# Kernel optimization log

Hardware: AMD Instinct MI355X
Metric: run time of the kernel (lower is better)

## Reference

```python
import jax, jax.numpy as jnp
import numpy as np


def setup_inputs() -> dict:
    key = jax.random.key(0)
    k_h, k_w1, k_w2 = jax.random.split(key, 3)
    B, S, D = 8, 2048, 1024
    H = 2 * D  # reasoning_net hidden width
    # xavier_uniform-style scaled weights
    lim1 = float(np.sqrt(6.0 / (D + H)))
    lim2 = float(np.sqrt(6.0 / (H + D)))
    return {
        "hidden_states": jax.random.normal(k_h, (B, S, D), dtype=jnp.float32),
        "W1": jax.random.uniform(k_w1, (D, H), dtype=jnp.float32, minval=-lim1, maxval=lim1),
        "b1": jnp.zeros((H,), dtype=jnp.float32),
        "W2": jax.random.uniform(k_w2, (H, D), dtype=jnp.float32, minval=-lim2, maxval=lim2),
        "b2": jnp.zeros((D,), dtype=jnp.float32),
    }


def reference(hidden_states, W1, b1, W2, b2):
    """Chain reasoning forward.

    The torch loop carries output[:, -1:], but reasoning_net is a per-token MLP
    (Linear over the last dim), so processed[:, -1:] == MLP(current token) and the
    carried state never influences appended outputs. Faithful closed form:
      out[:, 0]  = hidden_states[:, 0]
      out[:, i]  = MLP(hidden_states[:, i])  for i >= 1
    Dropout is identity (eval). GELU is exact (torch default).
    """
    rest = hidden_states[:, 1:, :]  # [B, S-1, D]
    h = jax.nn.gelu(jnp.einsum("bsd,dh->bsh", rest, W1) + b1, approximate=False)
    out_rest = jnp.einsum("bsh,hd->bsd", h, W2) + b2
    return jnp.concatenate([hidden_states[:, :1, :], out_rest], axis=1)
```

## Files before the change

kernel.cpp:

```cpp
#include <hip/hip_runtime.h>
#include <hip/hip_bf16.h>
#include <cstdint>
#include <cstddef>

typedef unsigned short u16;
typedef __attribute__((ext_vector_type(8))) __bf16 bf16x8;
typedef __attribute__((ext_vector_type(4))) float f32x4;

__device__ __forceinline__ void gload_lds16(const void* g, void* l) {
    __builtin_amdgcn_global_load_lds(
        (const __attribute__((address_space(1))) unsigned int*)g,
        (__attribute__((address_space(3))) unsigned int*)l,
        16, 0, 0);
}

__device__ __forceinline__ u16 f2bf(float f) {
    union { float f; unsigned int u; } v; v.f = f;
    unsigned int r = v.u + 0x7fffu + ((v.u >> 16) & 1u);
    return (u16)(r >> 16);
}

template <int GELU, int OUT_BF16>
__global__ void gemm_bt_bias_act(const u16* __restrict__ A,
                                 const u16* __restrict__ Bt,
                                 const float* __restrict__ bias,
                                 void* __restrict__ Cv,
                                 int M, int N, int K) {
    __shared__ u16 As[128 * 32];
    __shared__ u16 Bs[128 * 32];

    const int tid  = threadIdx.x;
    const int lane = tid & 63;
    const int wave = tid >> 6;
    const int wm   = (wave >> 1) * 64;
    const int wn   = (wave & 1) * 64;
    const int mrow = lane & 15;
    const int half = lane >> 4;

    const size_t ldb = (size_t)K * 2;
    const char* Ab = (const char*)(A + (size_t)blockIdx.x * 128 * K);
    const char* Bb = (const char*)(Bt + (size_t)blockIdx.y * 128 * K);

    const int lin0 = tid, lin1 = tid + 256;
    const size_t aoff0 = (size_t)(lin0 >> 2) * ldb + ((lin0 & 3) << 4);
    const size_t aoff1 = (size_t)(lin1 >> 2) * ldb + ((lin1 & 3) << 4);

    f32x4 acc[4][4];
#pragma unroll
    for (int i = 0; i < 4; ++i)
#pragma unroll
        for (int j = 0; j < 4; ++j) acc[i][j] = f32x4{0.f, 0.f, 0.f, 0.f};

    for (int k0 = 0; k0 < K; k0 += 32) {
        const size_t kb = (size_t)k0 * 2;
        gload_lds16(Ab + aoff0 + kb, (char*)As + lin0 * 16);
        gload_lds16(Ab + aoff1 + kb, (char*)As + lin1 * 16);
        gload_lds16(Bb + aoff0 + kb, (char*)Bs + lin0 * 16);
        gload_lds16(Bb + aoff1 + kb, (char*)Bs + lin1 * 16);
        __syncthreads();

        bf16x8 af[4], bfr[4];
#pragma unroll
        for (int t = 0; t < 4; ++t)
            af[t] = *(const bf16x8*)(As + (wm + t * 16 + mrow) * 32 + half * 8);
#pragma unroll
        for (int t = 0; t < 4; ++t)
            bfr[t] = *(const bf16x8*)(Bs + (wn + t * 16 + mrow) * 32 + half * 8);

#pragma unroll
        for (int mi = 0; mi < 4; ++mi)
#pragma unroll
            for (int ni = 0; ni < 4; ++ni)
                acc[mi][ni] = __builtin_amdgcn_mfma_f32_16x16x32_bf16(
                    af[mi], bfr[ni], acc[mi][ni], 0, 0, 0);
        __syncthreads();
    }

    const int row0 = blockIdx.x * 128 + wm + half * 4;
    const int col0 = blockIdx.y * 128 + wn + mrow;
#pragma unroll
    for (int ni = 0; ni < 4; ++ni) {
        const int col = col0 + ni * 16;
        const float bv = bias[col];
#pragma unroll
        for (int mi = 0; mi < 4; ++mi) {
            const int row = row0 + mi * 16;
#pragma unroll
            for (int r = 0; r < 4; ++r) {
                float v = acc[mi][ni][r] + bv;
                if (GELU) v = 0.5f * v * (1.0f + erff(v * 0.70710678118654752f));
                if (OUT_BF16)
                    ((u16*)Cv)[(size_t)(row + r) * N + col] = f2bf(v);
                else
                    ((float*)Cv)[(size_t)(row + r) * N + col] = v;
            }
        }
    }
}

__global__ void transpose_cvt_bf16(const float* __restrict__ src,
                                   u16* __restrict__ dst, int R, int C) {
    __shared__ u16 t[32][33];
    const int bx = blockIdx.x * 32;
    const int by = blockIdx.y * 32;
    const int x = threadIdx.x, y = threadIdx.y;
    for (int i = 0; i < 32; i += 8)
        t[y + i][x] = f2bf(src[(size_t)(by + y + i) * C + (bx + x)]);
    __syncthreads();
    for (int i = 0; i < 32; i += 8)
        dst[(size_t)(bx + y + i) * R + (by + x)] = t[x][y + i];
}

__global__ void cvt_bf16(const float* __restrict__ src, u16* __restrict__ dst,
                         long long n) {
    const long long i = ((long long)blockIdx.x * blockDim.x + threadIdx.x) * 4;
    if (i + 3 < n) {
        const float4 v = *(const float4*)(src + i);
        ushort4 o;
        o.x = f2bf(v.x); o.y = f2bf(v.y); o.z = f2bf(v.z); o.w = f2bf(v.w);
        *(ushort4*)(dst + i) = o;
    }
}

__global__ void fixup_first_token(const float* __restrict__ hs,
                                  float* __restrict__ out, int S, int D) {
    const size_t base = (size_t)blockIdx.x * S * D;
    for (int i = threadIdx.x; i < D; i += blockDim.x)
        out[base + i] = hs[base + i];
}

extern "C" void kernel_launch(void* const* d_in, const int* in_sizes, int n_in,
                              void* d_out, int out_size, void* d_ws, size_t ws_size,
                              hipStream_t stream) {
    const float* X  = (const float*)d_in[0];
    const float* W1 = (const float*)d_in[1];
    const float* b1 = (const float*)d_in[2];
    const float* W2 = (const float*)d_in[3];
    const float* b2 = (const float*)d_in[4];
    float* out = (float*)d_out;

    const int B = 8, S = 2048, D = 1024, H = 2048;
    const int M = B * S;

    u16* W1T = (u16*)d_ws;
    u16* W2T = W1T + (size_t)H * D;
    u16* Xb  = W2T + (size_t)D * H;
    const size_t wfixed = (size_t)H * D * 2 * 2;
    const size_t perrow = (size_t)(D + H) * 2;
    size_t avail_rows = (ws_size > wfixed) ? (ws_size - wfixed) / perrow : 0;
    int CM = (int)((avail_rows / 128) * 128);
    if (CM > M) CM = M;
    if (CM < 128) CM = 128;
    u16* Hb = Xb + (size_t)CM * D;

    dim3 tb(32, 8);
    transpose_cvt_bf16<<<dim3(H / 32, D / 32), tb, 0, stream>>>(W1, W1T, D, H);
    transpose_cvt_bf16<<<dim3(D / 32, H / 32), tb, 0, stream>>>(W2, W2T, H, D);

    for (int m0 = 0; m0 < M; m0 += CM) {
        const int rows = (M - m0 < CM) ? (M - m0) : CM;
        const long long n = (long long)rows * D;
        cvt_bf16<<<dim3((unsigned)(n / 1024)), dim3(256), 0, stream>>>(
            X + (size_t)m0 * D, Xb, n);
        dim3 g1(rows / 128, H / 128);
        gemm_bt_bias_act<1, 1><<<g1, dim3(256), 0, stream>>>(
            Xb, W1T, b1, Hb, rows, H, D);
        dim3 g2(rows / 128, D / 128);
        gemm_bt_bias_act<0, 0><<<g2, dim3(256), 0, stream>>>(
            Hb, W2T, b2, out + (size_t)m0 * D, rows, D, H);
    }

    fixup_first_token<<<dim3(B), dim3(256), 0, stream>>>(X, out, S, D);
}
```

Measured before the change: 328.6 us.

## Load A fragments directly from global, swizzle B in LDS, stage epilogue

The GEMM kernel now reads the A operand directly from global memory into registers. Only B goes through LDS, with an XOR swizzle meant to avoid bank conflicts. The epilogue writes results through an LDS tile so global stores are coalesced 16-byte vectors instead of scattered scalar writes. The exact erf GELU is replaced with a tanh approximation built on exp2/rcp intrinsics. The direct A loads are not shared between waves that use the same rows, which adds global traffic, and the tanh GELU changes numerics slightly.

```diff
diff --git a/kernel.cpp b/kernel.cpp
--- a/kernel.cpp
+++ b/kernel.cpp
@@ -5,6 +5,7 @@
 
 typedef unsigned short u16;
 typedef __attribute__((ext_vector_type(8))) __bf16 bf16x8;
+typedef __attribute__((ext_vector_type(8))) unsigned short u16x8;
 typedef __attribute__((ext_vector_type(4))) float f32x4;
 
 __device__ __forceinline__ void gload_lds16(const void* g, void* l) {
@@ -20,14 +21,22 @@
     return (u16)(r >> 16);
 }
 
+__device__ __forceinline__ float gelu_tanh(float x) {
+    const float z = 0.7978845608028654f * x * (1.0f + 0.044715f * x * x);
+    const float t = __builtin_amdgcn_exp2f(2.885390081777927f * z);
+    const float th = 1.0f - 2.0f * __builtin_amdgcn_rcpf(t + 1.0f);
+    return 0.5f * x * (1.0f + th);
+}
+
 template <int GELU, int OUT_BF16>
-__global__ void gemm_bt_bias_act(const u16* __restrict__ A,
-                                 const u16* __restrict__ Bt,
-                                 const float* __restrict__ bias,
-                                 void* __restrict__ Cv,
-                                 int M, int N, int K) {
-    __shared__ u16 As[128 * 32];
-    __shared__ u16 Bs[128 * 32];
+__global__ void gemm_adirect(const u16* __restrict__ A,
+                             const u16* __restrict__ Bt,
+                             const float* __restrict__ bias,
+                             void* __restrict__ Cv,
+                             int M, int N, int K) {
+    __shared__ __align__(16) char smem[16896];
+    u16* Bs = (u16*)smem;
+    float* Ct = (float*)smem;
 
     const int tid  = threadIdx.x;
     const int lane = tid & 63;
@@ -38,12 +47,26 @@
     const int half = lane >> 4;
 
     const size_t ldb = (size_t)K * 2;
-    const char* Ab = (const char*)(A + (size_t)blockIdx.x * 128 * K);
     const char* Bb = (const char*)(Bt + (size_t)blockIdx.y * 128 * K);
-
-    const int lin0 = tid, lin1 = tid + 256;
-    const size_t aoff0 = (size_t)(lin0 >> 2) * ldb + ((lin0 & 3) << 4);
-    const size_t aoff1 = (size_t)(lin1 >> 2) * ldb + ((lin1 & 3) << 4);
+    const char* Ab = (const char*)A;
+
+    const int r0 = tid >> 2, g0 = tid & 3;
+    const int r1 = r0 + 64;
+    const size_t boff0 = (size_t)r0 * ldb + (size_t)((g0 ^ ((r0 >> 1) & 3)) << 4);
+    const size_t boff1 = (size_t)r1 * ldb + (size_t)((g0 ^ ((r1 >> 1) & 3)) << 4);
+
+    size_t aoff[4];
+#pragma unroll
+    for (int mi = 0; mi < 4; ++mi)
+        aoff[mi] = ((size_t)(blockIdx.x * 128 + wm + mi * 16 + mrow)) * ldb
+                 + (size_t)(half << 4);
+
+    int blds[4];
+#pragma unroll
+    for (int t = 0; t < 4; ++t) {
+        const int rb = wn + t * 16 + mrow;
+        blds[t] = rb * 64 + ((half ^ ((rb >> 1) & 3)) << 4);
+    }
 
     f32x4 acc[4][4];
 #pragma unroll
@@ -53,47 +76,82 @@
 
     for (int k0 = 0; k0 < K; k0 += 32) {
         const size_t kb = (size_t)k0 * 2;
-        gload_lds16(Ab + aoff0 + kb, (char*)As + lin0 * 16);
-        gload_lds16(Ab + aoff1 + kb, (char*)As + lin1 * 16);
-        gload_lds16(Bb + aoff0 + kb, (char*)Bs + lin0 * 16);
-        gload_lds16(Bb + aoff1 + kb, (char*)Bs + lin1 * 16);
-        __syncthreads();
-
-        bf16x8 af[4], bfr[4];
+        gload_lds16(Bb + boff0 + kb, (char*)Bs + tid * 16);
+        gload_lds16(Bb + boff1 + kb, (char*)Bs + (tid + 256) * 16);
+
+        bf16x8 a[4];
+#pragma unroll
+        for (int mi = 0; mi < 4; ++mi)
+            a[mi] = *(const bf16x8*)(Ab + aoff[mi] + kb);
+
+        __syncthreads();
+
+        bf16x8 bfr[4];
 #pragma unroll
         for (int t = 0; t < 4; ++t)
-            af[t] = *(const bf16x8*)(As + (wm + t * 16 + mrow) * 32 + half * 8);
-#pragma unroll
-        for (int t = 0; t < 4; ++t)
-            bfr[t] = *(const bf16x8*)(Bs + (wn + t * 16 + mrow) * 32 + half * 8);
+            bfr[t] = *(const bf16x8*)((const char*)Bs + blds[t]);
 
 #pragma unroll
         for (int mi = 0; mi < 4; ++mi)
 #pragma unroll
             for (int ni = 0; ni < 4; ++ni)
                 acc[mi][ni] = __builtin_amdgcn_mfma_f32_16x16x32_bf16(
-                    af[mi], bfr[ni], acc[mi][ni], 0, 0, 0);
-        __syncthreads();
-    }
-
-    const int row0 = blockIdx.x * 128 + wm + half * 4;
-    const int col0 = blockIdx.y * 128 + wn + mrow;
-#pragma unroll
-    for (int ni = 0; ni < 4; ++ni) {
-        const int col = col0 + ni * 16;
-        const float bv = bias[col];
-#pragma unroll
-        for (int mi = 0; mi < 4; ++mi) {
-            const int row = row0 + mi * 16;
-#pragma unroll
-            for (int r = 0; r < 4; ++r) {
-                float v = acc[mi][ni][r] + bv;
-                if (GELU) v = 0.5f * v * (1.0f + erff(v * 0.70710678118654752f));
-                if (OUT_BF16)
-                    ((u16*)Cv)[(size_t)(row + r) * N + col] = f2bf(v);
-                else
-                    ((float*)Cv)[(size_t)(row + r) * N + col] = v;
+                    a[mi], bfr[ni], acc[mi][ni], 0, 0, 0);
+
+        __syncthreads();
+    }
+
+    const int lrow0 = wm + half * 4;
+    const int lcol0 = wn + mrow;
+    const int growbase = blockIdx.x * 128;
+    const int gcolbase = blockIdx.y * 128;
+    const int rr_rd = tid >> 3, cs_rd = (tid & 7) * 16;
+
+#pragma unroll
+    for (int c = 0; c < 4; ++c) {
+        __syncthreads();
+        if ((wm >> 6) == (c >> 1)) {
+            const int mi0 = (c & 1) * 2;
+#pragma unroll
+            for (int dmi = 0; dmi < 2; ++dmi) {
+                const int mi = mi0 + dmi;
+#pragma unroll
+                for (int ni = 0; ni < 4; ++ni) {
+                    const int col = lcol0 + ni * 16;
+                    const float bv = bias[gcolbase + col];
+#pragma unroll
+                    for (int r = 0; r < 4; ++r) {
+                        const int rr = (mi * 16 + lrow0 + r) & 31;
+                        float v = acc[mi][ni][r] + bv;
+                        if (GELU) v = gelu_tanh(v);
+                        Ct[rr * 132 + col] = v;
+                    }
+                }
             }
+        }
+        __syncthreads();
+        const float* ct = &Ct[rr_rd * 132 + cs_rd];
+        const f32x4 v0 = *(const f32x4*)(ct);
+        const f32x4 v1 = *(const f32x4*)(ct + 4);
+        const f32x4 v2 = *(const f32x4*)(ct + 8);
+        const f32x4 v3 = *(const f32x4*)(ct + 12);
+        const int grow = growbase + 32 * c + rr_rd;
+        if (OUT_BF16) {
+            u16x8 lo, hi;
+#pragma unroll
+            for (int j = 0; j < 4; ++j) {
+                lo[j] = f2bf(v0[j]); lo[j + 4] = f2bf(v1[j]);
+                hi[j] = f2bf(v2[j]); hi[j + 4] = f2bf(v3[j]);
+            }
+            u16* p = (u16*)Cv + (size_t)grow * N + gcolbase + cs_rd;
+            *(u16x8*)(p)     = lo;
+            *(u16x8*)(p + 8) = hi;
+        } else {
+            float* p = (float*)Cv + (size_t)grow * N + gcolbase + cs_rd;
+            *(f32x4*)(p)      = v0;
+            *(f32x4*)(p + 4)  = v1;
+            *(f32x4*)(p + 8)  = v2;
+            *(f32x4*)(p + 12) = v3;
         }
     }
 }
@@ -163,10 +221,10 @@
         cvt_bf16<<<dim3((unsigned)(n / 1024)), dim3(256), 0, stream>>>(
             X + (size_t)m0 * D, Xb, n);
         dim3 g1(rows / 128, H / 128);
-        gemm_bt_bias_act<1, 1><<<g1, dim3(256), 0, stream>>>(
+        gemm_adirect<1, 1><<<g1, dim3(256), 0, stream>>>(
             Xb, W1T, b1, Hb, rows, H, D);
         dim3 g2(rows / 128, D / 128);
-        gemm_bt_bias_act<0, 0><<<g2, dim3(256), 0, stream>>>(
+        gemm_adirect<0, 0><<<g2, dim3(256), 0, stream>>>(
             Hb, W2T, b2, out + (size_t)m0 * D, rows, D, H);
     }
 
```

Result: slower. 442.2 us (+34.6%).
